# Kernel tuning notes

Hardware: AMD Instinct MI355X
Metric: run time of the kernel (lower is better)

Reference implementation:

```python
import jax, jax.numpy as jnp
import numpy as np

IMG = 640.0  # pixel coordinate range for keypoints


def setup_inputs() -> dict:
    key = jax.random.key(0)
    ks = jax.random.split(key, 16)
    B, N, M, C, D, G = 4, 4096, 4096, 256, 256, 32
    s = 1.0 / np.sqrt(C)
    inp = {
        "nodes_t": jax.random.normal(ks[0], (B, N, C), jnp.float32),
        "nodes_t1": jax.random.normal(ks[1], (B, M, C), jnp.float32),
        "kpts_t1_pred": jax.random.uniform(ks[2], (B, N, 2), jnp.float32) * IMG,
        "kpts_t1_actual": jax.random.uniform(ks[3], (B, M, 2), jnp.float32) * IMG,
        "Wq": jax.random.normal(ks[4], (D, C), jnp.float32) * s,
        "bq": jnp.zeros((D,), jnp.float32),
        "Wk": jax.random.normal(ks[5], (D, C), jnp.float32) * s,
        "bk": jnp.zeros((D,), jnp.float32),
        "Wv": jax.random.normal(ks[6], (D, C), jnp.float32) * s,
        "bv": jnp.zeros((D,), jnp.float32),
        "Wm": jax.random.normal(ks[7], (D, D), jnp.float32) * (1.0 / np.sqrt(D)),
        "bm": jnp.zeros((D,), jnp.float32),
        "Wg1": jax.random.normal(ks[8], (G, 3), jnp.float32) * (1.0 / np.sqrt(3.0)),
        "bg1": jnp.zeros((G,), jnp.float32),
        "Wg2": jax.random.normal(ks[9], (G, G), jnp.float32) * (1.0 / np.sqrt(G)),
        "bg2": jnp.zeros((G,), jnp.float32),
        "iter_idx": 0,
    }
    return inp


def reference(nodes_t, nodes_t1, kpts_t1_pred, kpts_t1_actual,
              Wq, bq, Wk, bk, Wv, bv, Wm, bm, Wg1, bg1, Wg2, bg2, iter_idx):
    # window size schedule (iter_idx is a static Python int)
    win = 64.0 if iter_idx == 0 else max(4.0, 32.0 / 2 ** (iter_idx - 1))

    Q = nodes_t @ Wq.T + bq      # [B,N,256]
    K = nodes_t1 @ Wk.T + bk     # [B,M,256]
    V = nodes_t1 @ Wv.T + bv     # [B,M,256]

    # distance-based window mask [B,N,M]
    du = jnp.abs(kpts_t1_pred[:, :, 0:1] - kpts_t1_actual[:, None, :, 0])
    dv = jnp.abs(kpts_t1_pred[:, :, 1:2] - kpts_t1_actual[:, None, :, 1])
    mask = (du < win) & (dv < win)

    attn = jnp.einsum('bnd,bmd->bnm', Q, K) / jnp.sqrt(jnp.float32(256.0))
    attn = jnp.where(mask, attn, jnp.float32(-1e9))
    w = jax.nn.softmax(attn, axis=-1)

    matched_features = jnp.einsum('bnm,bmd->bnd', w, V)        # [B,N,256]
    matched_kpts = jnp.einsum('bnm,bmc->bnc', w, kpts_t1_actual)  # [B,N,2]

    confidence = jnp.any(mask, axis=-1, keepdims=True).astype(jnp.float32)  # [B,N,1]
    flow_residual = (matched_kpts - kpts_t1_pred) * confidence

    geo_in = jnp.concatenate([flow_residual, confidence], axis=-1)  # [B,N,3]
    h = jax.nn.silu(geo_in @ Wg1.T + bg1)
    geo_temp = h @ Wg2.T + bg2                                   # [B,N,32]

    merged = matched_features @ Wm.T + bm                        # [B,N,256]
    return merged, geo_temp, flow_residual, confidence
```

## Files before the change

kernel.cpp:

```cpp
#include <hip/hip_runtime.h>
#include <hip/hip_bf16.h>

typedef unsigned short ushort;
typedef unsigned int uint;
typedef __bf16 bf16x8 __attribute__((ext_vector_type(8)));
typedef float f32x4 __attribute__((ext_vector_type(4)));
typedef ushort ushort8 __attribute__((ext_vector_type(8)));

#define LOG2E 1.4426950408889634f
#define MFMA16(a,b,c) __builtin_amdgcn_mfma_f32_16x16x32_bf16((a),(b),(c),0,0,0)
#define GLL16(src, dst) __builtin_amdgcn_global_load_lds( \
    (const __attribute__((address_space(1))) void*)(src), \
    (__attribute__((address_space(3))) void*)(dst), 16, 0, 0)
#define GLL4(src, dst) __builtin_amdgcn_global_load_lds( \
    (const __attribute__((address_space(1))) void*)(src), \
    (__attribute__((address_space(3))) void*)(dst), 4, 0, 0)

static __device__ __forceinline__ uint packbf(float lo, float hi) {
  union { __bf16 h[2]; uint u; } x;
  x.h[0] = (__bf16)lo; x.h[1] = (__bf16)hi;
  return x.u;
}
static __device__ __forceinline__ int cellof(float x) {
  int c = (int)(x * 0.015625f);
  return c < 0 ? 0 : (c > 9 ? 9 : c);
}

__global__ __launch_bounds__(256) void prep_kernel(
    const float* __restrict__ Wq, const float* __restrict__ Wk,
    const float* __restrict__ Wv, const float* __restrict__ Wm,
    __bf16* __restrict__ wsW,
    const float* __restrict__ n0, const float* __restrict__ n1,
    __bf16* __restrict__ a0, __bf16* __restrict__ a1,
    const float* __restrict__ kpred, const float* __restrict__ kact,
    int* __restrict__ hist, int* __restrict__ cellpt,
    float* __restrict__ meanN)
{
  const int bid = blockIdx.x, tid = threadIdx.x;
  if (bid < 64) {
    const int which = bid >> 4;
    const float* src = which == 0 ? Wq : which == 1 ? Wk : which == 2 ? Wv : Wm;
    const int i = (bid & 15) * 4096 + tid * 16;
    #pragma unroll
    for (int j2 = 0; j2 < 4; j2++) {
      f32x4 v = *(const f32x4*)(src + i + j2 * 4);
      union { __bf16 h[4]; uint u[2]; } x;
      #pragma unroll
      for (int j = 0; j < 4; j++) x.h[j] = (__bf16)v[j];
      *(uint*)(wsW + (size_t)which * 65536 + i + j2 * 4) = x.u[0];
      *(uint*)(wsW + (size_t)which * 65536 + i + j2 * 4 + 2) = x.u[1];
    }
  } else if (bid < 8256) {
    const int k = bid - 64;
    const float* s = k < 4096 ? n0 : n1;
    __bf16* o = k < 4096 ? a0 : a1;
    const int i = (k & 4095) * 1024 + tid * 4;
    f32x4 v = *(const f32x4*)(s + i);
    union { __bf16 h[4]; uint u[2]; } x;
    #pragma unroll
    for (int j = 0; j < 4; j++) x.h[j] = (__bf16)v[j];
    *(uint*)(o + i) = x.u[0];
    *(uint*)(o + i + 2) = x.u[1];
  } else if (bid < 8384) {
    const int p = (bid - 8256) * 256 + tid;
    const int type = p >> 14, idx = p & 16383;
    const float2 c = ((const float2*)(type == 0 ? kpred : kact))[idx];
    const int cell = cellof(c.x) * 10 + cellof(c.y);
    const int b = idx >> 12;
    atomicAdd(&hist[(type * 4 + b) * 128 + cell], 1);
    cellpt[type * 16384 + idx] = cell;
  } else {
    const int mb = bid - 8384;
    const int b = mb >> 4, chunk = mb & 15;
    const float* base = n1 + ((size_t)b * 4096 + chunk * 256) * 256 + tid;
    float s = 0.f;
    for (int r = 0; r < 256; r++) s += base[(size_t)r * 256];
    atomicAdd(&meanN[b * 256 + tid], s);
  }
}

__global__ __launch_bounds__(256) void scan_vmean(
    const int* __restrict__ hist, int* __restrict__ strt, int* __restrict__ curs,
    const float* __restrict__ meanN, const float* __restrict__ Wv,
    const float* __restrict__ bv, float* __restrict__ Vmean)
{
  __shared__ int sh[1024];
  __shared__ float mn[256];
  const int t = threadIdx.x;
  if (blockIdx.x == 0) {
    for (int i = t; i < 1024; i += 256) sh[i] = hist[i];
    __syncthreads();
    if (t < 8) {
      int run = 0;
      for (int c = 0; c < 100; c++) {
        strt[t * 128 + c] = run;
        curs[t * 128 + c] = run;
        run += sh[t * 128 + c];
      }
      strt[t * 128 + 100] = run;
    }
  } else {
    const int b = blockIdx.x - 1;
    mn[t] = meanN[b * 256 + t] * (1.0f / 4096.0f);
    __syncthreads();
    float s = bv[t];
    const float* w = Wv + (size_t)t * 256;
    for (int c = 0; c < 256; c++) s += mn[c] * w[c];
    Vmean[b * 256 + t] = s;
  }
}

__global__ __launch_bounds__(256) void scatter_kernel(
    const float* __restrict__ kpred, const float* __restrict__ kact,
    const int* __restrict__ cellpt, int* __restrict__ curs,
    int* __restrict__ sq, int* __restrict__ invq, float* __restrict__ kpS,
    int* __restrict__ sk, int* __restrict__ invk, float* __restrict__ kaS)
{
  int p = blockIdx.x * 256 + threadIdx.x;
  int type = p >> 14, idx = p & 16383;
  int b = idx >> 12, n = idx & 4095;
  int cell = cellpt[type * 16384 + idx];
  int pos = atomicAdd(&curs[(type * 4 + b) * 128 + cell], 1);
  if (type == 0) {
    sq[b * 4096 + pos] = n;
    invq[b * 4096 + n] = pos;
    ((float2*)kpS)[b * 4096 + pos] = ((const float2*)kpred)[idx];
  } else {
    sk[b * 4096 + pos] = n;
    invk[b * 4096 + n] = pos;
    ((float2*)kaS)[b * 4096 + pos] = ((const float2*)kact)[idx];
  }
}

__global__ __launch_bounds__(256) void gemm_qkv(
    const ushort* __restrict__ A0, const ushort* __restrict__ A1,
    const ushort* __restrict__ W4,
    const float* __restrict__ bq, const float* __restrict__ bk,
    const float* __restrict__ bv,
    __bf16* __restrict__ outQ, __bf16* __restrict__ outK,
    __bf16* __restrict__ outVs,
    const int* __restrict__ invq, const int* __restrict__ invk)
{
  const int z = blockIdx.z;
  const ushort* A = z == 0 ? A0 : A1;
  const ushort* Wa = z == 0 ? W4 : W4 + 65536;
  const ushort* Wb = W4 + 131072;
  const int* inv = z == 0 ? invq : invk;

  const int wid = threadIdx.x >> 6;
  const int lane = threadIdx.x & 63;
  const int q = lane & 15, g = lane >> 4;
  const int nb = blockIdx.x * 64 + (wid >> 1) * 32;
  const int db = blockIdx.y * 128 + (wid & 1) * 64;

  f32x4 acc[2][4], accv[2][4];
  #pragma unroll
  for (int a = 0; a < 2; a++)
    #pragma unroll
    for (int b = 0; b < 4; b++) {
      acc[a][b] = f32x4{0.f,0.f,0.f,0.f};
      accv[a][b] = f32x4{0.f,0.f,0.f,0.f};
    }

  const ushort* Wa0 = Wa + (size_t)(db + q) * 256 + g * 8;
  const ushort* Wb0 = Wb + (size_t)(db + q) * 256 + g * 8;
  const ushort* Ar0 = A + (size_t)(nb + q) * 256 + g * 8;
  const ushort* Ar1 = A + (size_t)(nb + 16 + q) * 256 + g * 8;

  #pragma unroll
  for (int c0 = 0; c0 < 256; c0 += 32) {
    bf16x8 a0 = *(const bf16x8*)(Ar0 + c0);
    bf16x8 a1 = *(const bf16x8*)(Ar1 + c0);
    #pragma unroll
    for (int df = 0; df < 4; df++) {
      bf16x8 w = *(const bf16x8*)(Wa0 + df * 16 * 256 + c0);
      acc[0][df] = MFMA16(a0, w, acc[0][df]);
      acc[1][df] = MFMA16(a1, w, acc[1][df]);
    }
    if (z == 1) {
      #pragma unroll
      for (int df = 0; df < 4; df++) {
        bf16x8 w = *(const bf16x8*)(Wb0 + df * 16 * 256 + c0);
        accv[0][df] = MFMA16(a0, w, accv[0][df]);
        accv[1][df] = MFMA16(a1, w, accv[1][df]);
      }
    }
  }
  const float* biasA = z == 0 ? bq : bk;
  __bf16* oA = z == 0 ? outQ : outK;
  #pragma unroll
  for (int df = 0; df < 4; df++) {
    float ba = biasA[db + df * 16 + q];
    float bb = bv[db + df * 16 + q];
    #pragma unroll
    for (int nf = 0; nf < 2; nf++)
      #pragma unroll
      for (int r = 0; r < 4; r++) {
        int row = nb + nf * 16 + g * 4 + r;
        int d = db + df * 16 + q;
        int pos = inv[row];
        size_t orow = (size_t)(row & ~4095) + pos;
        oA[orow * 256 + d] = (__bf16)(acc[nf][df][r] + ba);
        if (z == 1)
          outVs[orow * 256 + d] = (__bf16)(accv[nf][df][r] + bb);
      }
  }
}

__global__ __launch_bounds__(256) void transpose_v(
    const ushort* __restrict__ Vs, ushort* __restrict__ VT)
{
  __shared__ ushort tile[64][76];
  const int b = blockIdx.z, rt = blockIdx.x, dt = blockIdx.y;
  const int tid = threadIdx.x;
  const ushort* src = Vs + ((size_t)b * 4096 + rt * 64) * 256 + dt * 64;
  #pragma unroll
  for (int i = 0; i < 2; i++) {
    int c = tid + i * 256;
    int r = c >> 3, dc = (c & 7) * 8;
    ushort8 v = *(const ushort8*)(src + (size_t)r * 256 + dc);
    #pragma unroll
    for (int j = 0; j < 8; j++) tile[r][dc + j] = v[j];
  }
  __syncthreads();
  ushort* dst = VT + ((size_t)b * 256 + dt * 64) * 4096 + rt * 64;
  #pragma unroll
  for (int i = 0; i < 2; i++) {
    int c = tid + i * 256;
    int d = c >> 3, rc = (c & 7) * 8;
    ushort8 v;
    #pragma unroll
    for (int j = 0; j < 8; j++) v[j] = tile[rc + j][d];
    *(ushort8*)(dst + (size_t)d * 4096 + rc) = v;
  }
}

__global__ __launch_bounds__(256, 2) void attn_kernel(
    const ushort* __restrict__ Q,
    const ushort* __restrict__ K,
    const ushort* __restrict__ VT,
    const float* __restrict__ kpS,
    const int* __restrict__ iter_idx,
    const int* __restrict__ sq,
    const int* __restrict__ strt,
    const float* __restrict__ kaS,
    const float* __restrict__ Vmean,
    __bf16* __restrict__ matched,
    float* __restrict__ out_flow, float* __restrict__ out_conf)
{
  __shared__ __align__(16) ushort Kl[2][8192];
  __shared__ __align__(16) ushort Vl[2][8192];
  __shared__ __align__(16) float2 Cl[2][32];
  __shared__ int tl_t[132], tl_ks[132], tl_ke[132];
  __shared__ int ntile_s;

  const int tid = threadIdx.x;
  const int wid = tid >> 6, lane = tid & 63;
  const int q = lane & 15, g = lane >> 4;
  const int orig = blockIdx.x;
  const int wgid = (orig & 7) * 50 + (orig >> 3);
  const int batch = wgid / 100;
  const int cell = wgid % 100;

  const int qstart = strt[batch * 128 + cell];
  const int nq = strt[batch * 128 + cell + 1] - qstart;
  if (nq == 0) return;

  const int cu = cell / 10, cv = cell % 10;
  const int c0 = cv > 0 ? cv - 1 : 0, c1 = cv < 9 ? cv + 1 : 9;
  const int* kst = strt + (4 + batch) * 128;

  if (tid == 0) {
    int n = 0;
    int lo = cu > 0 ? cu - 1 : 0, hi = cu < 9 ? cu + 1 : 9;
    for (int cc = lo; cc <= hi; cc++) {
      int ks = kst[cc * 10 + c0];
      int ke = kst[cc * 10 + c1 + 1];
      for (int t = ks & ~31; t < ke; t += 32) {
        tl_t[n] = t; tl_ks[n] = ks; tl_ke[n] = ke; n++;
      }
    }
    ntile_s = n;
  }
  __syncthreads();
  const int ntile = ntile_s;

  const int idx = *iter_idx;
  const float win = (idx == 0) ? 64.0f : fmaxf(4.0f, ldexpf(32.0f, 1 - idx));

  const ushort* Kbase = K + (size_t)batch * 4096 * 256;
  const ushort* VTb = VT + (size_t)batch * 1048576;
  const float* kasf = kaS + (size_t)batch * 8192;
  const float* Vm = Vmean + batch * 256;

  const int npass = (nq + 63) >> 6;

  auto STAGE = [&](int ti, int b) {
    const int t = tl_t[ti];
    #pragma unroll
    for (int j = 0; j < 4; j++) {
      int n = wid * 256 + j * 64 + lane;
      int r = n >> 5, u = n & 31;
      GLL16(Kbase + (size_t)(t + r) * 256 + ((u ^ (r & 7)) * 8),
            &Kl[b][(size_t)(wid * 256 + j * 64) * 8]);
    }
    #pragma unroll
    for (int j = 0; j < 4; j++) {
      int n = wid * 256 + j * 64 + lane;
      int d = n >> 2, c = n & 3;
      GLL16(VTb + (size_t)d * 4096 + t + ((c ^ ((d >> 1) & 3)) * 8),
            &Vl[b][(size_t)(wid * 256 + j * 64) * 8]);
    }
    if (wid == 0) GLL4(kasf + t * 2 + lane, &Cl[b][0]);
  };

  int cnt = 0, qi = 0;
  bool active = false;
  float pu = 0.f, pv = 0.f;
  bf16x8 qf[8];
  f32x4 O[16];
  float m_run = -1e9f, l_run = 0.f, u_run = 0.f, v_run = 0.f;

  auto PASS_INIT = [&](int pp) {
    int tbase = pp * 64 + wid * 16;
    active = tbase < nq;
    cnt = active ? min(16, nq - tbase) : 0;
    if (active) {
      int qq = q < cnt ? q : cnt - 1;
      int qsrow = batch * 4096 + qstart + tbase + qq;
      qi = sq[qsrow];
      const ushort* qptr = Q + (size_t)qsrow * 256 + g * 8;
      #pragma unroll
      for (int mf = 0; mf < 8; mf++) qf[mf] = *(const bf16x8*)(qptr + mf * 32);
      float2 kpv = ((const float2*)kpS)[qsrow];
      pu = kpv.x; pv = kpv.y;
    }
    #pragma unroll
    for (int i = 0; i < 16; i++) O[i] = f32x4{0.f,0.f,0.f,0.f};
    m_run = -1e9f; l_run = 0.f; u_run = 0.f; v_run = 0.f;
  };

  auto EPILOGUE = [&]() {
    if (!active) return;
    l_run += __shfl_xor(l_run, 16); l_run += __shfl_xor(l_run, 32);
    u_run += __shfl_xor(u_run, 16); u_run += __shfl_xor(u_run, 32);
    v_run += __shfl_xor(v_run, 16); v_run += __shfl_xor(v_run, 32);
    bool degen = (m_run <= -5e8f) || (l_run == 0.f);
    float rinv = degen ? 0.f : 1.0f / l_run;
    if (g == 0 && q < cnt) {
      float conf = degen ? 0.f : 1.0f;
      int row = batch * 4096 + qi;
      float fu = (u_run * rinv - pu) * conf, fv = (v_run * rinv - pv) * conf;
      ((float2*)out_flow)[row] = float2{fu, fv};
      out_conf[row] = conf;
    }
    #pragma unroll
    for (int r = 0; r < 4; r++) {
      int src = 4 * g + r;
      int qi_r = __shfl(qi, src);
      float il_r = __shfl(rinv, src);
      bool dg_r = (il_r == 0.f);
      if (src < cnt) {
        __bf16* mrow = matched + ((size_t)batch * 4096 + qi_r) * 256;
        #pragma unroll
        for (int df = 0; df < 16; df++) {
          float val = dg_r ? Vm[df * 16 + q] : O[df][r] * il_r;
          mrow[df * 16 + q] = (__bf16)val;
        }
      }
    }
  };

  if (ntile == 0) {
    for (int pp = 0; pp < npass; pp++) { PASS_INIT(pp); EPILOGUE(); }
    return;
  }

  const int total = npass * ntile;
  STAGE(0, 0);
  PASS_INIT(0);

  int i = 0, pp = 0;
  for (int it = 0; it < total; ++it) {
    __syncthreads();
    if (it + 1 < total) {
      int ni = (i + 1 == ntile) ? 0 : i + 1;
      STAGE(ni, (it + 1) & 1);
    }
    const int b = it & 1;

    if (active) {
      const int t = tl_t[i], ks = tl_ks[i], ke = tl_ke[i];

      f32x4 s0a = {0.f,0.f,0.f,0.f}, s0b = {0.f,0.f,0.f,0.f};
      f32x4 s1a = {0.f,0.f,0.f,0.f}, s1b = {0.f,0.f,0.f,0.f};
      #pragma unroll
      for (int mf = 0; mf < 8; mf += 2) {
        const int u0 = (mf * 4 + g) ^ (q & 7);
        const int u1 = ((mf + 1) * 4 + g) ^ (q & 7);
        bf16x8 ka0 = *(const bf16x8*)&Kl[b][(size_t)(q * 32 + u0) * 8];
        bf16x8 kb0 = *(const bf16x8*)&Kl[b][(size_t)(q * 32 + u1) * 8];
        bf16x8 ka1 = *(const bf16x8*)&Kl[b][(size_t)((q + 16) * 32 + u0) * 8];
        bf16x8 kb1 = *(const bf16x8*)&Kl[b][(size_t)((q + 16) * 32 + u1) * 8];
        s0a = MFMA16(ka0, qf[mf],     s0a);
        s0b = MFMA16(kb0, qf[mf + 1], s0b);
        s1a = MFMA16(ka1, qf[mf],     s1a);
        s1b = MFMA16(kb1, qf[mf + 1], s1b);
      }

      float aus[8], avs[8], sv[8];
      #pragma unroll
      for (int r = 0; r < 4; r++) {
        int jr = t + 4 * g + r;
        float2 cc0 = Cl[b][4 * g + r];
        aus[r] = cc0.x; avs[r] = cc0.y;
        bool val = (jr >= ks && jr < ke);
        float du = fabsf(pu - cc0.x), dv = fabsf(pv - cc0.y);
        float sr = s0a[r] + s0b[r];
        sv[r] = (val && fmaxf(du, dv) < win) ? sr * 0.0625f : -1e9f;

        int jr1 = jr + 16;
        float2 cc1 = Cl[b][16 + 4 * g + r];
        aus[4 + r] = cc1.x; avs[4 + r] = cc1.y;
        val = (jr1 >= ks && jr1 < ke);
        du = fabsf(pu - cc1.x); dv = fabsf(pv - cc1.y);
        sr = s1a[r] + s1b[r];
        sv[4 + r] = (val && fmaxf(du, dv) < win) ? sr * 0.0625f : -1e9f;
      }

      float mt = fmaxf(fmaxf(fmaxf(sv[0], sv[1]), fmaxf(sv[2], sv[3])),
                       fmaxf(fmaxf(sv[4], sv[5]), fmaxf(sv[6], sv[7])));
      mt = fmaxf(mt, __shfl_xor(mt, 16));
      mt = fmaxf(mt, __shfl_xor(mt, 32));
      if (__any(mt > m_run + 8.0f)) {
        float m_new = fmaxf(m_run, mt);
        float scale = exp2f((m_run - m_new) * LOG2E);
        l_run *= scale; u_run *= scale; v_run *= scale;
        float s_r[4];
        #pragma unroll
        for (int r = 0; r < 4; r++) s_r[r] = __shfl(scale, 4 * g + r);
        #pragma unroll
        for (int df = 0; df < 16; df++)
          #pragma unroll
          for (int r = 0; r < 4; r++) O[df][r] *= s_r[r];
        m_run = m_new;
      }

      float p[8];
      #pragma unroll
      for (int ii = 0; ii < 8; ii++) p[ii] = exp2f((sv[ii] - m_run) * LOG2E);
      #pragma unroll
      for (int ii = 0; ii < 8; ii++) {
        l_run += p[ii];
        u_run += p[ii] * aus[ii];
        v_run += p[ii] * avs[ii];
      }

      uint d0 = packbf(p[0], p[1]), d1 = packbf(p[2], p[3]);
      uint d2 = packbf(p[4], p[5]), d3 = packbf(p[6], p[7]);
      int srcA = q + ((g & 1) << 5);
      int srcB = srcA + 16;
      uint x0 = (uint)__shfl((int)d0, srcA), x1 = (uint)__shfl((int)d1, srcA);
      uint x2 = (uint)__shfl((int)d0, srcB), x3 = (uint)__shfl((int)d1, srcB);
      uint y0 = (uint)__shfl((int)d2, srcA), y1 = (uint)__shfl((int)d3, srcA);
      uint y2 = (uint)__shfl((int)d2, srcB), y3 = (uint)__shfl((int)d3, srcB);
      union { uint i4[4]; bf16x8 v; } af;
      bool lo = (g < 2);
      af.i4[0] = lo ? x0 : y0; af.i4[1] = lo ? x1 : y1;
      af.i4[2] = lo ? x2 : y2; af.i4[3] = lo ? x3 : y3;

      const int vs = g ^ ((q >> 1) & 3);
      #pragma unroll
      for (int df = 0; df < 16; df++) {
        bf16x8 vfd = *(const bf16x8*)&Vl[b][(size_t)((df * 16 + q) * 4 + vs) * 8];
        O[df] = MFMA16(af.v, vfd, O[df]);
      }
    }

    if (i == ntile - 1) {
      EPILOGUE();
      pp++;
      if (pp < npass) PASS_INIT(pp);
      i = 0;
    } else {
      i++;
    }
  }
}

__global__ __launch_bounds__(256) void merged_geo(
    const ushort* __restrict__ A, const ushort* __restrict__ W,
    const float* __restrict__ bias, float* __restrict__ out,
    const float* __restrict__ flow, const float* __restrict__ conf_in,
    const float* __restrict__ Wg1, const float* __restrict__ bg1,
    const float* __restrict__ Wg2, const float* __restrict__ bg2,
    float* __restrict__ out_geo)
{
  __shared__ float w1[32][3], b1[32], b2[32];
  __shared__ __align__(16) float w2[32][32];
  if (blockIdx.x < 512) {
    const int wid = threadIdx.x >> 6;
    const int lane = threadIdx.x & 63;
    const int q = lane & 15, g = lane >> 4;
    const int nb = (blockIdx.x >> 1) * 64 + (wid >> 1) * 32;
    const int db = (blockIdx.x & 1) * 128 + (wid & 1) * 64;

    f32x4 acc[2][4];
    #pragma unroll
    for (int a = 0; a < 2; a++)
      #pragma unroll
      for (int b = 0; b < 4; b++) acc[a][b] = f32x4{0.f,0.f,0.f,0.f};

    const ushort* W0 = W + (size_t)(db + q) * 256 + g * 8;
    const ushort* Ar0 = A + (size_t)(nb + q) * 256 + g * 8;
    const ushort* Ar1 = A + (size_t)(nb + 16 + q) * 256 + g * 8;

    #pragma unroll
    for (int c0 = 0; c0 < 256; c0 += 32) {
      bf16x8 a0 = *(const bf16x8*)(Ar0 + c0);
      bf16x8 a1 = *(const bf16x8*)(Ar1 + c0);
      #pragma unroll
      for (int df = 0; df < 4; df++) {
        bf16x8 w = *(const bf16x8*)(W0 + df * 16 * 256 + c0);
        acc[0][df] = MFMA16(a0, w, acc[0][df]);
        acc[1][df] = MFMA16(a1, w, acc[1][df]);
      }
    }
    #pragma unroll
    for (int df = 0; df < 4; df++) {
      float bval = bias[db + df * 16 + q];
      #pragma unroll
      for (int nf = 0; nf < 2; nf++)
        #pragma unroll
        for (int r = 0; r < 4; r++) {
          int row = nb + nf * 16 + g * 4 + r;
          out[(size_t)row * 256 + db + df * 16 + q] = acc[nf][df][r] + bval;
        }
    }
  } else {
    const int tid = threadIdx.x;
    for (int i = tid; i < 96; i += 256) w1[i / 3][i % 3] = Wg1[i];
    if (tid < 32) { b1[tid] = bg1[tid]; b2[tid] = bg2[tid]; }
    for (int i = tid; i < 1024; i += 256) w2[i / 32][i % 32] = Wg2[i];
    __syncthreads();

    int row = (blockIdx.x - 512) * 256 + tid;
    float2 f = ((const float2*)flow)[row];
    float c = conf_in[row];
    float h[32];
    #pragma unroll
    for (int j = 0; j < 32; j++) {
      float x = w1[j][0] * f.x + w1[j][1] * f.y + w1[j][2] * c + b1[j];
      h[j] = x / (1.f + __expf(-x));
    }
    #pragma unroll
    for (int o = 0; o < 32; o += 2) {
      float s0 = b2[o], s1 = b2[o + 1];
      #pragma unroll
      for (int j = 0; j < 32; j += 4) {
        f32x4 wa = *(const f32x4*)&w2[o][j];
        f32x4 wb = *(const f32x4*)&w2[o + 1][j];
        s0 += wa[0]*h[j] + wa[1]*h[j+1] + wa[2]*h[j+2] + wa[3]*h[j+3];
        s1 += wb[0]*h[j] + wb[1]*h[j+1] + wb[2]*h[j+2] + wb[3]*h[j+3];
      }
      ((float2*)out_geo)[((size_t)row * 32 + o) >> 1] = float2{s0, s1};
    }
  }
}

extern "C" void kernel_launch(void* const* d_in, const int* in_sizes, int n_in,
                              void* d_out, int out_size, void* d_ws, size_t ws_size,
                              hipStream_t stream) {
  const float* nodes_t  = (const float*)d_in[0];
  const float* nodes_t1 = (const float*)d_in[1];
  const float* kpred    = (const float*)d_in[2];
  const float* kact     = (const float*)d_in[3];
  const float* Wq = (const float*)d_in[4];  const float* bq = (const float*)d_in[5];
  const float* Wk = (const float*)d_in[6];  const float* bk = (const float*)d_in[7];
  const float* Wv = (const float*)d_in[8];  const float* bv = (const float*)d_in[9];
  const float* Wm = (const float*)d_in[10]; const float* bm = (const float*)d_in[11];
  const float* Wg1= (const float*)d_in[12]; const float* bg1= (const float*)d_in[13];
  const float* Wg2= (const float*)d_in[14]; const float* bg2= (const float*)d_in[15];
  const int* iter = (const int*)d_in[16];

  float* out_merged = (float*)d_out;
  float* out_geo  = out_merged + 4 * 4096 * 256;
  float* out_flow = out_geo + 4 * 4096 * 32;
  float* out_conf = out_flow + 4 * 4096 * 2;

  ushort* wsQ   = (ushort*)d_ws;
  ushort* wsK   = wsQ + 4194304;
  ushort* wsVT  = wsK + 4194304;
  ushort* wsM   = wsVT + 4194304;
  ushort* wsW   = wsM + 4194304;
  float*  kaS   = (float*)(wsW + 262144);
  float*  kpS   = kaS + 32768;
  float*  Vmean = kpS + 32768;
  int*    hist  = (int*)(Vmean + 1024);
  float*  meanN = (float*)(hist + 1024);
  int*    strt  = (int*)(meanN + 1024);
  int*    curs  = strt + 1024;
  int*    cellpt= curs + 1024;
  int*    sq    = cellpt + 32768;
  int*    sk    = sq + 16384;
  int*    invk  = sk + 16384;
  int*    invq  = invk + 16384;
  ushort* wsA0  = (ushort*)(invq + 16384);
  ushort* wsA1  = wsA0 + 4194304;

  hipMemsetAsync(hist, 0, 8192, stream);

  prep_kernel<<<8448, 256, 0, stream>>>(Wq, Wk, Wv, Wm, (__bf16*)wsW,
                                        nodes_t, nodes_t1,
                                        (__bf16*)wsA0, (__bf16*)wsA1,
                                        kpred, kact, hist, cellpt, meanN);
  scan_vmean<<<5, 256, 0, stream>>>(hist, strt, curs, meanN, Wv, bv, Vmean);
  scatter_kernel<<<128, 256, 0, stream>>>(kpred, kact, cellpt, curs,
                                          sq, invq, kpS, sk, invk, kaS);
  dim3 qg(256, 2, 2);
  gemm_qkv<<<qg, 256, 0, stream>>>(wsA0, wsA1, wsW, bq, bk, bv,
                                   (__bf16*)wsQ, (__bf16*)wsK, (__bf16*)wsM,
                                   invq, invk);
  dim3 tg(64, 4, 4);
  transpose_v<<<tg, 256, 0, stream>>>(wsM, wsVT);
  attn_kernel<<<400, 256, 0, stream>>>(wsQ, wsK, wsVT, kpS, iter,
                                       sq, strt, kaS, Vmean,
                                       (__bf16*)wsM, out_flow, out_conf);
  merged_geo<<<576, 256, 0, stream>>>(wsM, wsW + 196608, bm, out_merged,
                                      out_flow, out_conf,
                                      Wg1, bg1, Wg2, bg2, out_geo);
}
```

Measured before the change: 180.0 us.

## Split K/V staging with two barriers per tile, write matched rows sorted order

```diff
diff --git a/kernel.cpp b/kernel.cpp
--- a/kernel.cpp
+++ b/kernel.cpp
@@ -15,6 +15,7 @@
 #define GLL4(src, dst) __builtin_amdgcn_global_load_lds( \
     (const __attribute__((address_space(1))) void*)(src), \
     (__attribute__((address_space(3))) void*)(dst), 4, 0, 0)
+#define SCHED0() __builtin_amdgcn_sched_barrier(0)
 
 static __device__ __forceinline__ uint packbf(float lo, float hi) {
   union { __bf16 h[2]; uint u; } x;
@@ -295,7 +296,7 @@
 
   const int npass = (nq + 63) >> 6;
 
-  auto STAGE = [&](int ti, int b) {
+  auto STAGE_K = [&](int ti, int b) {
     const int t = tl_t[ti];
     #pragma unroll
     for (int j = 0; j < 4; j++) {
@@ -304,6 +305,10 @@
       GLL16(Kbase + (size_t)(t + r) * 256 + ((u ^ (r & 7)) * 8),
             &Kl[b][(size_t)(wid * 256 + j * 64) * 8]);
     }
+    if (wid == 0) GLL4(kasf + t * 2 + lane, &Cl[b][0]);
+  };
+  auto STAGE_V = [&](int ti, int b) {
+    const int t = tl_t[ti];
     #pragma unroll
     for (int j = 0; j < 4; j++) {
       int n = wid * 256 + j * 64 + lane;
@@ -311,10 +316,9 @@
       GLL16(VTb + (size_t)d * 4096 + t + ((c ^ ((d >> 1) & 3)) * 8),
             &Vl[b][(size_t)(wid * 256 + j * 64) * 8]);
     }
-    if (wid == 0) GLL4(kasf + t * 2 + lane, &Cl[b][0]);
   };
 
-  int cnt = 0, qi = 0;
+  int cnt = 0, qi = 0, qbase_s = 0;
   bool active = false;
   float pu = 0.f, pv = 0.f;
   bf16x8 qf[8];
@@ -325,9 +329,10 @@
     int tbase = pp * 64 + wid * 16;
     active = tbase < nq;
     cnt = active ? min(16, nq - tbase) : 0;
+    qbase_s = batch * 4096 + qstart + tbase;
     if (active) {
       int qq = q < cnt ? q : cnt - 1;
-      int qsrow = batch * 4096 + qstart + tbase + qq;
+      int qsrow = qbase_s + qq;
       qi = sq[qsrow];
       const ushort* qptr = Q + (size_t)qsrow * 256 + g * 8;
       #pragma unroll
@@ -356,12 +361,11 @@
     }
     #pragma unroll
     for (int r = 0; r < 4; r++) {
-      int src = 4 * g + r;
-      int qi_r = __shfl(qi, src);
-      float il_r = __shfl(rinv, src);
+      int slot = 4 * g + r;
+      float il_r = __shfl(rinv, slot);
       bool dg_r = (il_r == 0.f);
-      if (src < cnt) {
-        __bf16* mrow = matched + ((size_t)batch * 4096 + qi_r) * 256;
+      if (slot < cnt) {
+        __bf16* mrow = matched + (size_t)(qbase_s + slot) * 256;
         #pragma unroll
         for (int df = 0; df < 16; df++) {
           float val = dg_r ? Vm[df * 16 + q] : O[df][r] * il_r;
@@ -377,23 +381,31 @@
   }
 
   const int total = npass * ntile;
-  STAGE(0, 0);
+  STAGE_K(0, 0);
+  STAGE_V(0, 0);
   PASS_INIT(0);
 
   int i = 0, pp = 0;
   for (int it = 0; it < total; ++it) {
-    __syncthreads();
-    if (it + 1 < total) {
-      int ni = (i + 1 == ntile) ? 0 : i + 1;
-      STAGE(ni, (it + 1) & 1);
-    }
     const int b = it & 1;
+    const int ni = (i + 1 == ntile) ? 0 : i + 1;
+    const bool more = (it + 1 < total);
+    const int nb = (it + 1) & 1;
+
+    asm volatile("s_waitcnt vmcnt(4)" ::: "memory");
+    SCHED0();
+    __builtin_amdgcn_s_barrier();
+    SCHED0();
+    if (more) STAGE_K(ni, nb);
+
+    const int t = tl_t[i], ks = tl_ks[i], ke = tl_ke[i];
+    float sv[8], aus[8], avs[8];
+    uint pp0 = 0, pp1 = 0, pp2 = 0, pp3 = 0;
 
     if (active) {
-      const int t = tl_t[i], ks = tl_ks[i], ke = tl_ke[i];
-
       f32x4 s0a = {0.f,0.f,0.f,0.f}, s0b = {0.f,0.f,0.f,0.f};
       f32x4 s1a = {0.f,0.f,0.f,0.f}, s1b = {0.f,0.f,0.f,0.f};
+      __builtin_amdgcn_s_setprio(1);
       #pragma unroll
       for (int mf = 0; mf < 8; mf += 2) {
         const int u0 = (mf * 4 + g) ^ (q & 7);
@@ -407,8 +419,8 @@
         s1a = MFMA16(ka1, qf[mf],     s1a);
         s1b = MFMA16(kb1, qf[mf + 1], s1b);
       }
-
-      float aus[8], avs[8], sv[8];
+      __builtin_amdgcn_s_setprio(0);
+
       #pragma unroll
       for (int r = 0; r < 4; r++) {
         int jr = t + 4 * g + r;
@@ -455,26 +467,37 @@
         u_run += p[ii] * aus[ii];
         v_run += p[ii] * avs[ii];
       }
-
-      uint d0 = packbf(p[0], p[1]), d1 = packbf(p[2], p[3]);
-      uint d2 = packbf(p[4], p[5]), d3 = packbf(p[6], p[7]);
+      pp0 = packbf(p[0], p[1]); pp1 = packbf(p[2], p[3]);
+      pp2 = packbf(p[4], p[5]); pp3 = packbf(p[6], p[7]);
+    }
+
+    if (more) { asm volatile("s_waitcnt vmcnt(4)" ::: "memory"); }
+    else      { asm volatile("s_waitcnt vmcnt(0)" ::: "memory"); }
+    SCHED0();
+    __builtin_amdgcn_s_barrier();
+    SCHED0();
+    if (more) STAGE_V(ni, nb);
+
+    if (active) {
       int srcA = q + ((g & 1) << 5);
       int srcB = srcA + 16;
-      uint x0 = (uint)__shfl((int)d0, srcA), x1 = (uint)__shfl((int)d1, srcA);
-      uint x2 = (uint)__shfl((int)d0, srcB), x3 = (uint)__shfl((int)d1, srcB);
-      uint y0 = (uint)__shfl((int)d2, srcA), y1 = (uint)__shfl((int)d3, srcA);
-      uint y2 = (uint)__shfl((int)d2, srcB), y3 = (uint)__shfl((int)d3, srcB);
+      uint x0 = (uint)__shfl((int)pp0, srcA), x1 = (uint)__shfl((int)pp1, srcA);
+      uint x2 = (uint)__shfl((int)pp0, srcB), x3 = (uint)__shfl((int)pp1, srcB);
+      uint y0 = (uint)__shfl((int)pp2, srcA), y1 = (uint)__shfl((int)pp3, srcA);
+      uint y2 = (uint)__shfl((int)pp2, srcB), y3 = (uint)__shfl((int)pp3, srcB);
       union { uint i4[4]; bf16x8 v; } af;
       bool lo = (g < 2);
       af.i4[0] = lo ? x0 : y0; af.i4[1] = lo ? x1 : y1;
       af.i4[2] = lo ? x2 : y2; af.i4[3] = lo ? x3 : y3;
 
       const int vs = g ^ ((q >> 1) & 3);
+      __builtin_amdgcn_s_setprio(1);
       #pragma unroll
       for (int df = 0; df < 16; df++) {
         bf16x8 vfd = *(const bf16x8*)&Vl[b][(size_t)((df * 16 + q) * 4 + vs) * 8];
         O[df] = MFMA16(af.v, vfd, O[df]);
       }
+      __builtin_amdgcn_s_setprio(0);
     }
 
     if (i == ntile - 1) {
@@ -491,6 +514,7 @@
 __global__ __launch_bounds__(256) void merged_geo(
     const ushort* __restrict__ A, const ushort* __restrict__ W,
     const float* __restrict__ bias, float* __restrict__ out,
+    const int* __restrict__ sq,
     const float* __restrict__ flow, const float* __restrict__ conf_in,
     const float* __restrict__ Wg1, const float* __restrict__ bg1,
     const float* __restrict__ Wg2, const float* __restrict__ bg2,
@@ -534,7 +558,8 @@
         #pragma unroll
         for (int r = 0; r < 4; r++) {
           int row = nb + nf * 16 + g * 4 + r;
-          out[(size_t)row * 256 + db + df * 16 + q] = acc[nf][df][r] + bval;
+          int orow = (row & ~4095) + sq[row];
+          out[(size_t)orow * 256 + db + df * 16 + q] = acc[nf][df][r] + bval;
         }
     }
   } else {
@@ -626,7 +651,7 @@
   attn_kernel<<<400, 256, 0, stream>>>(wsQ, wsK, wsVT, kpS, iter,
                                        sq, strt, kaS, Vmean,
                                        (__bf16*)wsM, out_flow, out_conf);
-  merged_geo<<<576, 256, 0, stream>>>(wsM, wsW + 196608, bm, out_merged,
+  merged_geo<<<576, 256, 0, stream>>>(wsM, wsW + 196608, bm, out_merged, sq,
                                       out_flow, out_conf,
                                       Wg1, bg1, Wg2, bg2, out_geo);
 }
```

Result: slower. 185.2 us (+2.9%).
